# Performance work log

Hardware: AMD Instinct MI355X
Metric: run time of the kernel (lower is better)

The kernel has to match this reference:

```python
import jax, jax.numpy as jnp
import numpy as np

D_MODEL = 1024
N_HEADS = 16
D_K = D_MODEL // N_HEADS
THETA = 10000.0
B, S = 4, 2048


def _rope(x, positions):
    # x: [B, H, S, D_K]; positions: [S] int
    half = D_K // 2
    inv_freq = THETA ** (-jnp.arange(0, half, dtype=jnp.float32) * 2.0 / D_K)  # [half]
    ang = positions.astype(jnp.float32)[:, None] * inv_freq[None, :]  # [S, half]
    cos = jnp.cos(ang)[None, None, :, :]
    sin = jnp.sin(ang)[None, None, :, :]
    x_even = x[..., 0::2]
    x_odd = x[..., 1::2]
    out_even = x_even * cos - x_odd * sin
    out_odd = x_even * sin + x_odd * cos
    # interleave back to original layout
    out = jnp.stack([out_even, out_odd], axis=-1).reshape(x.shape)
    return out


def setup_inputs() -> dict:
    key = jax.random.key(0)
    ks = jax.random.split(key, 5)
    scale = 1.0 / np.sqrt(D_MODEL)
    return {
        "x": jax.random.normal(ks[0], (B, S, D_MODEL), dtype=jnp.float32),
        "token_positions": jnp.arange(S, dtype=jnp.int64 if jax.config.jax_enable_x64 else jnp.int32),
        "Wq": jax.random.normal(ks[1], (D_MODEL, D_MODEL), dtype=jnp.float32) * scale,
        "Wk": jax.random.normal(ks[2], (D_MODEL, D_MODEL), dtype=jnp.float32) * scale,
        "Wv": jax.random.normal(ks[3], (D_MODEL, D_MODEL), dtype=jnp.float32) * scale,
        "Wo": jax.random.normal(ks[4], (D_MODEL, D_MODEL), dtype=jnp.float32) * scale,
    }


def reference(x, token_positions, Wq, Wk, Wv, Wo):
    bsz, seq_len, _ = x.shape
    # projections (Linear_Transform: y = x @ W^T, no bias)
    def proj(W):
        h = jnp.einsum("bsd,ed->bse", x, W)
        return h.reshape(bsz, seq_len, N_HEADS, D_K).transpose(0, 2, 1, 3)  # [B,H,S,Dk]
    Q = proj(Wq)
    K = proj(Wk)
    V = proj(Wv)
    Q = _rope(Q, token_positions)
    K = _rope(K, token_positions)
    # scaled dot product attention with causal mask
    scores = jnp.einsum("bhqd,bhkd->bhqk", Q, K) / jnp.sqrt(jnp.float32(D_K))
    causal = jnp.tril(jnp.ones((seq_len, seq_len), dtype=bool))  # [S,S]
    scores = jnp.where(causal[None, None, :, :], scores, -jnp.inf)
    attn = jax.nn.softmax(scores, axis=-1)
    out = jnp.einsum("bhqk,bhkd->bhqd", attn, V)
    out = out.transpose(0, 2, 1, 3).reshape(bsz, seq_len, D_MODEL)
    return jnp.einsum("bsd,ed->bse", out, Wo)
```

## Files before the change

kernel.cpp:

```cpp
#include <hip/hip_runtime.h>
#include <hip/hip_bf16.h>
#include <cstdint>
#include <cstddef>

typedef __attribute__((ext_vector_type(4))) float f32x4;
typedef __attribute__((ext_vector_type(16))) float f32x16;
typedef __attribute__((ext_vector_type(8))) short bf16x8;
typedef unsigned int u32;
typedef unsigned short u16;


__device__ __forceinline__ u16 f2bf(float x) {
  u32 u = __builtin_bit_cast(u32, x);
  u += 0x7fffu + ((u >> 16) & 1u);
  return (u16)(u >> 16);
}

__device__ __forceinline__ u32 cvt_pk_bf16(float lo, float hi) {
  u32 r;
  asm("v_cvt_pk_bf16_f32 %0, %1, %2" : "=v"(r) : "v"(lo), "v"(hi));
  return r;
}

__device__ __forceinline__ float fexp2(float x) {
  float r;
  asm("v_exp_f32 %0, %1\n\ts_nop 1" : "=v"(r) : "v"(x));
  return r;
}

__device__ __forceinline__ void perm_swap(u32& a, u32& b) {
  asm("v_permlane32_swap_b32 %0, %1" : "+v"(a), "+v"(b));
}

__device__ __forceinline__ void gl_lds16(const void* g, void* l) {
  __builtin_amdgcn_global_load_lds(
      (const __attribute__((address_space(1))) u32*)(uintptr_t)g,
      (__attribute__((address_space(3))) u32*)(u32)(uintptr_t)l,
      16, 0, 0);
}

#define MFMA16(a, b, c) __builtin_amdgcn_mfma_f32_16x16x32_bf16((a), (b), (c), 0, 0, 0)
#define MFMA32(a, b, c) __builtin_amdgcn_mfma_f32_32x32x16_bf16((a), (b), (c), 0, 0, 0)


__global__ void cast_all_k(const float* __restrict__ x, const float* __restrict__ wq,
                           const float* __restrict__ wk, const float* __restrict__ wv,
                           const float* __restrict__ wo, u16* __restrict__ xb,
                           u16* __restrict__ wqb, u16* __restrict__ wkb,
                           u16* __restrict__ wvb, u16* __restrict__ wob) {
  int blk = blockIdx.x;
  const float* s; u16* d; int i;
  if (blk < 8192)       { s = x;  d = xb;  i = blk * 256; }
  else if (blk < 9216)  { s = wq; d = wqb; i = (blk - 8192) * 256; }
  else if (blk < 10240) { s = wk; d = wkb; i = (blk - 9216) * 256; }
  else if (blk < 11264) { s = wv; d = wvb; i = (blk - 10240) * 256; }
  else                  { s = wo; d = wob; i = (blk - 11264) * 256; }
  i += threadIdx.x;
  const float4 v = reinterpret_cast<const float4*>(s)[i];
  uint2 o;
  o.x = cvt_pk_bf16(v.x, v.y);
  o.y = cvt_pk_bf16(v.z, v.w);
  reinterpret_cast<uint2*>(d)[i] = o;
}


__global__ void rope_table_k(const int* __restrict__ pos, float2* __restrict__ cs) {
  int idx = blockIdx.x * 256 + threadIdx.x;
  int s = idx >> 5, i = idx & 31;
  float inv = powf(10000.0f, -(float)i * (1.0f / 32.0f));
  float ang = (float)pos[s] * inv;
  cs[idx] = float2{cosf(ang), sinf(ang)};
}


__global__ __launch_bounds__(256, 2)
void gemm_qkv(const u16* __restrict__ A, const u16* __restrict__ B,
              const float2* __restrict__ cs, u16* __restrict__ Qr,
              u16* __restrict__ Kr, u16* __restrict__ Vt, float qscale) {
  const int K = 1024;
  __shared__ u16 a_lds[2][128 * 32];
  __shared__ u16 b_lds[2][128 * 32];
  const int tid = threadIdx.x;
  const int l = tid & 63;
  const int w = tid >> 6;
  const int wm = w >> 1, wn = w & 1;
  const int bm = blockIdx.y, bn = blockIdx.x;

  const u16* Ab = A + (size_t)bm * 128 * K;
  const u16* Bb = B + (size_t)bn * 128 * K;

  auto stage = [&](int bq, int k0) {
#pragma unroll
    for (int half = 0; half < 2; ++half) {
      int t = half * 256 + tid;
      int row = t >> 2, slot = t & 3;
      int sp = slot ^ ((row >> 1) & 3);
      gl_lds16(Ab + (size_t)row * K + k0 + sp * 8, &a_lds[bq][t * 8]);
      gl_lds16(Bb + (size_t)row * K + k0 + sp * 8, &b_lds[bq][t * 8]);
    }
  };

  const f32x4 fz = {0.f, 0.f, 0.f, 0.f};
  f32x4 acc[4][4];
#pragma unroll
  for (int mi = 0; mi < 4; ++mi)
#pragma unroll
    for (int ni = 0; ni < 4; ++ni) acc[mi][ni] = fz;

  const int nk = K >> 5;
  stage(0, 0);
  int buf = 0;
  for (int kt = 0; kt < nk; ++kt) {
    __syncthreads();
    if (kt + 1 < nk) stage(buf ^ 1, (kt + 1) * 32);
    bf16x8 af[4], bf[4];
#pragma unroll
    for (int mi = 0; mi < 4; ++mi) {
      int row = wm * 64 + mi * 16 + (l & 15);
      int sp = (l >> 4) ^ ((row >> 1) & 3);
      af[mi] = *(const bf16x8*)&a_lds[buf][row * 32 + sp * 8];
    }
#pragma unroll
    for (int ni = 0; ni < 4; ++ni) {
      int row = wn * 64 + ni * 16 + (l & 15);
      int sp = (l >> 4) ^ ((row >> 1) & 3);
      bf[ni] = *(const bf16x8*)&b_lds[buf][row * 32 + sp * 8];
    }
#pragma unroll
    for (int mi = 0; mi < 4; ++mi)
#pragma unroll
      for (int ni = 0; ni < 4; ++ni)
        acc[mi][ni] = MFMA16(af[mi], bf[ni], acc[mi][ni]);
    buf ^= 1;
  }

  const int sector = bn >> 3;
  const int colb = ((bn & 7) << 7) + wn * 64;
  const int c = l & 15, h4 = l >> 4;

  if (sector == 2) {
#pragma unroll
    for (int mi = 0; mi < 4; ++mi) {
      int row = bm * 128 + wm * 64 + mi * 16 + 4 * h4;
      int b_ = row >> 11, s = row & 2047;
#pragma unroll
      for (int ni = 0; ni < 4; ++ni) {
        int cv = colb + ni * 16 + c;
        int hh = cv >> 6, dk = cv & 63;
        f32x4 v = acc[mi][ni];
        uint2 st;
        st.x = cvt_pk_bf16(v[0], v[1]);
        st.y = cvt_pk_bf16(v[2], v[3]);
        *(uint2*)&Vt[(((size_t)b_ * 16 + hh) << 17) + ((size_t)dk << 11) + s] = st;
      }
    }
  } else {
    u16* dst = sector ? Kr : Qr;
    const float scale = sector ? 1.0f : qscale;
#pragma unroll
    for (int mi = 0; mi < 4; ++mi) {
      int row0 = bm * 128 + wm * 64 + mi * 16 + 4 * h4;
#pragma unroll
      for (int ni = 0; ni < 4; ++ni) {
        int cv = colb + ni * 16 + c;
        int hh = cv >> 6, i2 = cv & 63;
        f32x4 v = acc[mi][ni];
        f32x4 pv;
#pragma unroll
        for (int j = 0; j < 4; ++j) pv[j] = __shfl_xor(v[j], 1);
        if (!(l & 1)) {
#pragma unroll
          for (int j = 0; j < 4; ++j) {
            int r = row0 + j, s = r & 2047, b_ = r >> 11;
            float2 t = cs[(s << 5) + (i2 >> 1)];
            float oe = (v[j] * t.x - pv[j] * t.y) * scale;
            float oo = (v[j] * t.y + pv[j] * t.x) * scale;
            *(u32*)&dst[(((size_t)(b_ * 16 + hh) * 2048 + s) << 6) + i2] =
                cvt_pk_bf16(oe, oo);
          }
        }
      }
    }
  }
}


__global__ __launch_bounds__(256, 2)
void gemm_bt(const u16* __restrict__ A, const u16* __restrict__ B,
             float* __restrict__ C, int M, int N, int K) {
  __shared__ u16 a_lds[2][128 * 32];
  __shared__ u16 b_lds[2][128 * 32];
  const int tid = threadIdx.x;
  const int l = tid & 63;
  const int w = tid >> 6;
  const int wm = w >> 1, wn = w & 1;
  const int bm = blockIdx.y, bn = blockIdx.x;

  const u16* Ab = A + (size_t)bm * 128 * K;
  const u16* Bb = B + (size_t)bn * 128 * K;

  auto stage = [&](int bq, int k0) {
#pragma unroll
    for (int half = 0; half < 2; ++half) {
      int t = half * 256 + tid;
      int row = t >> 2, slot = t & 3;
      int sp = slot ^ ((row >> 1) & 3);
      gl_lds16(Ab + (size_t)row * K + k0 + sp * 8, &a_lds[bq][t * 8]);
      gl_lds16(Bb + (size_t)row * K + k0 + sp * 8, &b_lds[bq][t * 8]);
    }
  };

  const f32x4 fz = {0.f, 0.f, 0.f, 0.f};
  f32x4 acc[4][4];
#pragma unroll
  for (int mi = 0; mi < 4; ++mi)
#pragma unroll
    for (int ni = 0; ni < 4; ++ni) acc[mi][ni] = fz;

  const int nk = K >> 5;
  stage(0, 0);
  int buf = 0;
  for (int kt = 0; kt < nk; ++kt) {
    __syncthreads();
    if (kt + 1 < nk) stage(buf ^ 1, (kt + 1) * 32);
    bf16x8 af[4], bf[4];
#pragma unroll
    for (int mi = 0; mi < 4; ++mi) {
      int row = wm * 64 + mi * 16 + (l & 15);
      int sp = (l >> 4) ^ ((row >> 1) & 3);
      af[mi] = *(const bf16x8*)&a_lds[buf][row * 32 + sp * 8];
    }
#pragma unroll
    for (int ni = 0; ni < 4; ++ni) {
      int row = wn * 64 + ni * 16 + (l & 15);
      int sp = (l >> 4) ^ ((row >> 1) & 3);
      bf[ni] = *(const bf16x8*)&b_lds[buf][row * 32 + sp * 8];
    }
#pragma unroll
    for (int mi = 0; mi < 4; ++mi)
#pragma unroll
      for (int ni = 0; ni < 4; ++ni)
        acc[mi][ni] = MFMA16(af[mi], bf[ni], acc[mi][ni]);
    buf ^= 1;
  }

#pragma unroll
  for (int mi = 0; mi < 4; ++mi) {
    int rbase = bm * 128 + wm * 64 + mi * 16 + ((l >> 4) << 2);
#pragma unroll
    for (int ni = 0; ni < 4; ++ni) {
      int col = bn * 128 + wn * 64 + ni * 16 + (l & 15);
      f32x4 v = acc[mi][ni];
#pragma unroll
      for (int j = 0; j < 4; ++j)
        C[(size_t)(rbase + j) * N + col] = v[j];
    }
  }
}


__global__ __launch_bounds__(256, 2)
void attn_k(const u16* __restrict__ Q, const u16* __restrict__ K,
            const u16* __restrict__ V, u16* __restrict__ O) {
  const int S = 2048;
  __shared__ u16 k_lds[3][64 * 64];
  __shared__ u16 v_lds[3][64 * 64];

  const int tid = threadIdx.x, l = tid & 63, w = tid >> 6;
  const int lane31 = l & 31, hi = l >> 5;

  const int wg = blockIdx.x;
  const int idx = (wg & 7) * 64 + (wg >> 3);
  const int bh = idx >> 3, pairI = idx & 7;

  const u16* Kb = K + (size_t)bh * S * 64;
  const u16* Vb = V + (size_t)bh * 64 * S;
  const int b = bh >> 4, hd = bh & 15;

  auto stageKV = [&](int bq, int kv0) {
#pragma unroll
    for (int half = 0; half < 2; ++half) {
      int t = half * 256 + tid;
      int row = t >> 3, slot = t & 7;
      int sp = slot ^ (row & 7);
      gl_lds16(Kb + (size_t)(kv0 + row) * 64 + sp * 8, &k_lds[bq][t * 8]);
      gl_lds16(Vb + (size_t)row * S + kv0 + sp * 8, &v_lds[bq][t * 8]);
    }
  };

#pragma unroll 1
  for (int ph = 0; ph < 2; ++ph) {
    const int qi = ph ? (15 - pairI) : pairI;
    const int q0 = qi * 128;
    const int nkv = 2 * qi + 2;
    const int qrow = q0 + w * 32 + lane31;
    const u16* Qp = Q + ((size_t)bh * S + qrow) * 64;

    bf16x8 qf[4];
#pragma unroll
    for (int ks = 0; ks < 4; ++ks)
      qf[ks] = *(const bf16x8*)(Qp + ks * 16 + hi * 8);
    __builtin_amdgcn_sched_barrier(0);
    stageKV(0, 0);
    stageKV(1, 64);

    f32x16 oacc[2];
#pragma unroll
    for (int dt = 0; dt < 2; ++dt)
#pragma unroll
      for (int r = 0; r < 16; ++r) oacc[dt][r] = 0.f;
    float m_run = -1e30f, l_run = 0.f;

    int buf = 0;
#pragma unroll 1
    for (int t = 0; t < nkv; ++t) {
      if (t + 2 < nkv) {
        int b2 = buf + 2; if (b2 >= 3) b2 -= 3;
        stageKV(b2, (t + 2) * 64);
        __builtin_amdgcn_sched_barrier(0);
        asm volatile("s_waitcnt vmcnt(8)" ::: "memory");
      } else if (t + 1 < nkv) {
        asm volatile("s_waitcnt vmcnt(4)" ::: "memory");
      } else {
        asm volatile("s_waitcnt vmcnt(0)" ::: "memory");
      }
      __builtin_amdgcn_sched_barrier(0);
      __builtin_amdgcn_s_barrier();
      __builtin_amdgcn_sched_barrier(0);

      f32x16 sc[2];
#pragma unroll
      for (int dt = 0; dt < 2; ++dt)
#pragma unroll
        for (int r = 0; r < 16; ++r) sc[dt][r] = 0.f;
      __builtin_amdgcn_s_setprio(1);
#pragma unroll
      for (int ks = 0; ks < 4; ++ks) {
        int sp = (2 * ks + hi) ^ (lane31 & 7);
#pragma unroll
        for (int dt = 0; dt < 2; ++dt) {
          bf16x8 kf = *(const bf16x8*)&k_lds[buf][(dt * 32 + lane31) * 64 + sp * 8];
          sc[dt] = MFMA32(kf, qf[ks], sc[dt]);
        }
      }
      __builtin_amdgcn_s_setprio(0);

      bf16x8 vf[2][4];
#pragma unroll
      for (int ks = 0; ks < 4; ++ks) {
        int sp = (2 * ks + hi) ^ (lane31 & 7);
#pragma unroll
        for (int dt = 0; dt < 2; ++dt)
          vf[dt][ks] = *(const bf16x8*)&v_lds[buf][(dt * 32 + lane31) * 64 + sp * 8];
      }

      if (t >= nkv - 2) {
#pragma unroll
        for (int dt = 0; dt < 2; ++dt)
#pragma unroll
          for (int r = 0; r < 16; ++r) {
            int kvg = t * 64 + dt * 32 + (r & 3) + 8 * (r >> 2) + 4 * hi;
            if (kvg > qrow) sc[dt][r] = -1e30f;
          }
      }

      float r16[16];
#pragma unroll
      for (int i = 0; i < 16; ++i) r16[i] = fmaxf(sc[0][i], sc[1][i]);
#pragma unroll
      for (int i = 0; i < 8; ++i) r16[i] = fmaxf(r16[i], r16[i + 8]);
#pragma unroll
      for (int i = 0; i < 4; ++i) r16[i] = fmaxf(r16[i], r16[i + 4]);
      float mx = fmaxf(fmaxf(r16[0], r16[1]), fmaxf(r16[2], r16[3]));
      mx = fmaxf(mx, __shfl_xor(mx, 32));

      const bool nores = __all(mx <= m_run);
      float mnew = nores ? m_run : fmaxf(m_run, mx);
#pragma unroll
      for (int dt = 0; dt < 2; ++dt)
#pragma unroll
        for (int r = 0; r < 16; ++r) sc[dt][r] = fexp2(sc[dt][r] - mnew);
      float s16[16];
#pragma unroll
      for (int i = 0; i < 16; ++i) s16[i] = sc[0][i] + sc[1][i];
#pragma unroll
      for (int i = 0; i < 8; ++i) s16[i] += s16[i + 8];
#pragma unroll
      for (int i = 0; i < 4; ++i) s16[i] += s16[i + 4];
      float ps = (s16[0] + s16[1]) + (s16[2] + s16[3]);
      ps += __shfl_xor(ps, 32);

      if (nores) {
        l_run += ps;
      } else {
        float alpha = fexp2(m_run - mnew);
        l_run = l_run * alpha + ps;
        m_run = mnew;
#pragma unroll
        for (int dt = 0; dt < 2; ++dt)
#pragma unroll
          for (int r = 0; r < 16; ++r) oacc[dt][r] *= alpha;
      }

      union { u32 u[4]; bf16x8 v; } pf[4];
#pragma unroll
      for (int ks = 0; ks < 4; ++ks) {
        const int sidx = ks >> 1, rb = (ks & 1) * 8;
        u32 c01 = cvt_pk_bf16(sc[sidx][rb + 0], sc[sidx][rb + 1]);
        u32 c23 = cvt_pk_bf16(sc[sidx][rb + 2], sc[sidx][rb + 3]);
        u32 c45 = cvt_pk_bf16(sc[sidx][rb + 4], sc[sidx][rb + 5]);
        u32 c67 = cvt_pk_bf16(sc[sidx][rb + 6], sc[sidx][rb + 7]);
        perm_swap(c01, c45);
        perm_swap(c23, c67);
        pf[ks].u[0] = c01; pf[ks].u[1] = c23; pf[ks].u[2] = c45; pf[ks].u[3] = c67;
      }

      __builtin_amdgcn_s_setprio(1);
#pragma unroll
      for (int dt = 0; dt < 2; ++dt)
#pragma unroll
        for (int ks = 0; ks < 4; ++ks)
          oacc[dt] = MFMA32(vf[dt][ks], pf[ks].v, oacc[dt]);
      __builtin_amdgcn_s_setprio(0);

      buf = (buf == 2) ? 0 : buf + 1;
    }

    __builtin_amdgcn_sched_barrier(0);
    __builtin_amdgcn_s_barrier();
    __builtin_amdgcn_sched_barrier(0);

    float inv = 1.f / l_run;
    u16* Ob = O + (((size_t)(b * 2048 + qrow)) << 10) + hd * 64;
#pragma unroll
    for (int dt = 0; dt < 2; ++dt)
#pragma unroll
      for (int g = 0; g < 4; ++g) {
        uint2 st;
        st.x = cvt_pk_bf16(oacc[dt][4 * g + 0] * inv, oacc[dt][4 * g + 1] * inv);
        st.y = cvt_pk_bf16(oacc[dt][4 * g + 2] * inv, oacc[dt][4 * g + 3] * inv);
        *(uint2*)&Ob[dt * 32 + g * 8 + hi * 4] = st;
      }
  }
}


extern "C" void kernel_launch(void* const* d_in, const int* in_sizes, int n_in,
                              void* d_out, int out_size, void* d_ws, size_t ws_size,
                              hipStream_t stream) {
  (void)in_sizes; (void)n_in; (void)out_size; (void)ws_size;
  const float* x  = (const float*)d_in[0];
  const int* pos  = (const int*)d_in[1];
  const float* Wq = (const float*)d_in[2];
  const float* Wk = (const float*)d_in[3];
  const float* Wv = (const float*)d_in[4];
  const float* Wo = (const float*)d_in[5];
  float* out = (float*)d_out;

  const int S = 2048, D = 1024;
  const size_t M = (size_t)4 * S;

  char* ws = (char*)d_ws;
  size_t off = 0;
  auto alloc = [&](size_t bytes) {
    void* p = ws + off;
    off += (bytes + 255) & ~(size_t)255;
    return p;
  };
  u16* xb   = (u16*)alloc(M * D * 2);
  u16* wqb  = (u16*)alloc((size_t)D * D * 2);
  u16* wkb  = (u16*)alloc((size_t)D * D * 2);
  u16* wvb  = (u16*)alloc((size_t)D * D * 2);
  u16* wob  = (u16*)alloc((size_t)D * D * 2);
  u16* Qr   = (u16*)alloc(M * D * 2);
  u16* Kr   = (u16*)alloc(M * D * 2);
  u16* Vt   = (u16*)alloc(M * D * 2);
  u16* Ob   = (u16*)alloc(M * D * 2);
  float2* csT = (float2*)alloc((size_t)S * 32 * 8);

  cast_all_k<<<12288, 256, 0, stream>>>(x, Wq, Wk, Wv, Wo, xb, wqb, wkb, wvb, wob);
  rope_table_k<<<(S * 32) / 256, 256, 0, stream>>>(pos, csT);

  const float QSCALE = 0.125f * 1.4426950408889634f;

  gemm_qkv<<<dim3(24, (unsigned)(M / 128)), 256, 0, stream>>>(
      xb, wqb, csT, Qr, Kr, Vt, QSCALE);
  attn_k<<<512, 256, 0, stream>>>(Qr, Kr, Vt, Ob);
  gemm_bt<<<dim3(8, (unsigned)(M / 128)), 256, 0, stream>>>(Ob, wob, out, (int)M, D, D);
}
```

Before: 181.9 us.

## Enlarge QKV GEMM tile to 256x256 with 512 threads and triple-buffered loads

The fused QKV projection GEMM moves from 128x128 tiles with 256 threads and double buffering to 256x256 tiles with 512 threads (8 waves as 2x4), a three-slot LDS ring with explicit vmcnt waits, and raised wave priority around the MFMA block. Larger tiles raise arithmetic intensity and cut global and LDS traffic per FLOP. Prefetching two stages ahead is meant to hide load latency. The cost is fewer blocks (384 at one block per CU, so low occupancy and possible tail imbalance), 96KB of LDS and twice the accumulator registers per wave.

```diff
diff --git a/kernel.cpp b/kernel.cpp
--- a/kernel.cpp
+++ b/kernel.cpp
@@ -41,6 +41,8 @@
 
 #define MFMA16(a, b, c) __builtin_amdgcn_mfma_f32_16x16x32_bf16((a), (b), (c), 0, 0, 0)
 #define MFMA32(a, b, c) __builtin_amdgcn_mfma_f32_32x32x16_bf16((a), (b), (c), 0, 0, 0)
+#define SBAR() do { __builtin_amdgcn_sched_barrier(0); __builtin_amdgcn_s_barrier(); \
+                    __builtin_amdgcn_sched_barrier(0); } while (0)
 
 
 __global__ void cast_all_k(const float* __restrict__ x, const float* __restrict__ wq,
@@ -73,75 +75,91 @@
 }
 
 
-__global__ __launch_bounds__(256, 2)
+__global__ __launch_bounds__(512, 1)
 void gemm_qkv(const u16* __restrict__ A, const u16* __restrict__ B,
               const float2* __restrict__ cs, u16* __restrict__ Qr,
               u16* __restrict__ Kr, u16* __restrict__ Vt, float qscale) {
   const int K = 1024;
-  __shared__ u16 a_lds[2][128 * 32];
-  __shared__ u16 b_lds[2][128 * 32];
-  const int tid = threadIdx.x;
-  const int l = tid & 63;
-  const int w = tid >> 6;
-  const int wm = w >> 1, wn = w & 1;
+  __shared__ u16 a_lds[3][256 * 32];
+  __shared__ u16 b_lds[3][256 * 32];
+
+  const int tid = threadIdx.x, l = tid & 63;
+  const int wid = tid >> 6;
+  const int wr = wid >> 2, wc = wid & 3;
   const int bm = blockIdx.y, bn = blockIdx.x;
-
-  const u16* Ab = A + (size_t)bm * 128 * K;
-  const u16* Bb = B + (size_t)bn * 128 * K;
-
-  auto stage = [&](int bq, int k0) {
-#pragma unroll
-    for (int half = 0; half < 2; ++half) {
-      int t = half * 256 + tid;
-      int row = t >> 2, slot = t & 3;
+  const int c = l & 15, h4 = l >> 4;
+
+  const u16* Ab = A + (size_t)bm * 256 * K;
+  const u16* Bb = B + (size_t)bn * 256 * K;
+
+  auto stageT = [&](int sl, int k0) {
+#pragma unroll
+    for (int ch = 0; ch < 2; ++ch) {
+      int t5 = ch * 512 + tid;
+      int row = t5 >> 2, slot = t5 & 3;
       int sp = slot ^ ((row >> 1) & 3);
-      gl_lds16(Ab + (size_t)row * K + k0 + sp * 8, &a_lds[bq][t * 8]);
-      gl_lds16(Bb + (size_t)row * K + k0 + sp * 8, &b_lds[bq][t * 8]);
+      gl_lds16(Ab + (size_t)row * K + k0 + sp * 8, &a_lds[sl][t5 * 8]);
+      gl_lds16(Bb + (size_t)row * K + k0 + sp * 8, &b_lds[sl][t5 * 8]);
     }
   };
 
   const f32x4 fz = {0.f, 0.f, 0.f, 0.f};
-  f32x4 acc[4][4];
-#pragma unroll
-  for (int mi = 0; mi < 4; ++mi)
+  f32x4 acc[8][4];
+#pragma unroll
+  for (int mi = 0; mi < 8; ++mi)
 #pragma unroll
     for (int ni = 0; ni < 4; ++ni) acc[mi][ni] = fz;
 
   const int nk = K >> 5;
-  stage(0, 0);
-  int buf = 0;
-  for (int kt = 0; kt < nk; ++kt) {
-    __syncthreads();
-    if (kt + 1 < nk) stage(buf ^ 1, (kt + 1) * 32);
-    bf16x8 af[4], bf[4];
-#pragma unroll
-    for (int mi = 0; mi < 4; ++mi) {
-      int row = wm * 64 + mi * 16 + (l & 15);
-      int sp = (l >> 4) ^ ((row >> 1) & 3);
-      af[mi] = *(const bf16x8*)&a_lds[buf][row * 32 + sp * 8];
+  stageT(0, 0);
+  stageT(1, 32);
+
+  int sl = 0;
+#pragma unroll 1
+  for (int t = 0; t < nk; ++t) {
+    if (t + 2 < nk) {
+      int s2 = sl + 2; if (s2 >= 3) s2 -= 3;
+      stageT(s2, (t + 2) * 32);
+      __builtin_amdgcn_sched_barrier(0);
+      asm volatile("s_waitcnt vmcnt(8)" ::: "memory");
+    } else if (t + 1 < nk) {
+      asm volatile("s_waitcnt vmcnt(4)" ::: "memory");
+    } else {
+      asm volatile("s_waitcnt vmcnt(0)" ::: "memory");
+    }
+    SBAR();
+
+    bf16x8 af[8], bf[4];
+#pragma unroll
+    for (int mi = 0; mi < 8; ++mi) {
+      int row = wr * 128 + mi * 16 + c;
+      int sp = h4 ^ ((row >> 1) & 3);
+      af[mi] = *(const bf16x8*)&a_lds[sl][row * 32 + sp * 8];
     }
 #pragma unroll
     for (int ni = 0; ni < 4; ++ni) {
-      int row = wn * 64 + ni * 16 + (l & 15);
-      int sp = (l >> 4) ^ ((row >> 1) & 3);
-      bf[ni] = *(const bf16x8*)&b_lds[buf][row * 32 + sp * 8];
-    }
-#pragma unroll
-    for (int mi = 0; mi < 4; ++mi)
+      int row = wc * 64 + ni * 16 + c;
+      int sp = h4 ^ ((row >> 1) & 3);
+      bf[ni] = *(const bf16x8*)&b_lds[sl][row * 32 + sp * 8];
+    }
+    __builtin_amdgcn_s_setprio(1);
+#pragma unroll
+    for (int mi = 0; mi < 8; ++mi)
 #pragma unroll
       for (int ni = 0; ni < 4; ++ni)
         acc[mi][ni] = MFMA16(af[mi], bf[ni], acc[mi][ni]);
-    buf ^= 1;
+    __builtin_amdgcn_s_setprio(0);
+
+    sl = (sl == 2) ? 0 : sl + 1;
   }
 
-  const int sector = bn >> 3;
-  const int colb = ((bn & 7) << 7) + wn * 64;
-  const int c = l & 15, h4 = l >> 4;
+  const int sector = bn >> 2;
+  const int colb = ((bn & 3) << 8) + wc * 64;
 
   if (sector == 2) {
 #pragma unroll
-    for (int mi = 0; mi < 4; ++mi) {
-      int row = bm * 128 + wm * 64 + mi * 16 + 4 * h4;
+    for (int mi = 0; mi < 8; ++mi) {
+      int row = bm * 256 + wr * 128 + mi * 16 + 4 * h4;
       int b_ = row >> 11, s = row & 2047;
 #pragma unroll
       for (int ni = 0; ni < 4; ++ni) {
@@ -158,8 +176,8 @@
     u16* dst = sector ? Kr : Qr;
     const float scale = sector ? 1.0f : qscale;
 #pragma unroll
-    for (int mi = 0; mi < 4; ++mi) {
-      int row0 = bm * 128 + wm * 64 + mi * 16 + 4 * h4;
+    for (int mi = 0; mi < 8; ++mi) {
+      int row0 = bm * 256 + wr * 128 + mi * 16 + 4 * h4;
 #pragma unroll
       for (int ni = 0; ni < 4; ++ni) {
         int cv = colb + ni * 16 + c;
@@ -172,9 +190,9 @@
 #pragma unroll
           for (int j = 0; j < 4; ++j) {
             int r = row0 + j, s = r & 2047, b_ = r >> 11;
-            float2 t = cs[(s << 5) + (i2 >> 1)];
-            float oe = (v[j] * t.x - pv[j] * t.y) * scale;
-            float oo = (v[j] * t.y + pv[j] * t.x) * scale;
+            float2 tt = cs[(s << 5) + (i2 >> 1)];
+            float oe = (v[j] * tt.x - pv[j] * tt.y) * scale;
+            float oo = (v[j] * tt.y + pv[j] * tt.x) * scale;
             *(u32*)&dst[(((size_t)(b_ * 16 + hh) * 2048 + s) << 6) + i2] =
                 cvt_pk_bf16(oe, oo);
           }
@@ -324,9 +342,7 @@
       } else {
         asm volatile("s_waitcnt vmcnt(0)" ::: "memory");
       }
-      __builtin_amdgcn_sched_barrier(0);
-      __builtin_amdgcn_s_barrier();
-      __builtin_amdgcn_sched_barrier(0);
+      SBAR();
 
       f32x16 sc[2];
 #pragma unroll
@@ -426,9 +442,7 @@
       buf = (buf == 2) ? 0 : buf + 1;
     }
 
-    __builtin_amdgcn_sched_barrier(0);
-    __builtin_amdgcn_s_barrier();
-    __builtin_amdgcn_sched_barrier(0);
+    SBAR();
 
     float inv = 1.f / l_run;
     u16* Ob = O + (((size_t)(b * 2048 + qrow)) << 10) + hd * 64;
@@ -483,8 +497,7 @@
 
   const float QSCALE = 0.125f * 1.4426950408889634f;
 
-  gemm_qkv<<<dim3(24, (unsigned)(M / 128)), 256, 0, stream>>>(
-      xb, wqb, csT, Qr, Kr, Vt, QSCALE);
+  gemm_qkv<<<dim3(12, 32), 512, 0, stream>>>(xb, wqb, csT, Qr, Kr, Vt, QSCALE);
   attn_k<<<512, 256, 0, stream>>>(Qr, Kr, Vt, Ob);
   gemm_bt<<<dim3(8, (unsigned)(M / 128)), 256, 0, stream>>>(Ob, wob, out, (int)M, D, D);
 }
```

Result: slower. 185.7 us (+2.1%).
